# Optimization experiments

Hardware: AMD Instinct MI355X
Metric: run time of the kernel (lower is better)

Reference implementation:

```python
import jax, jax.numpy as jnp
import numpy as np

Z_DIMS = (64, 64, 64, 64)
B, T = 16, 1024
IN_CH, CH = 512, 2048
M = 1024
D = sum(Z_DIMS)
LN_EPS = 1e-5
COMMIT = 0.25


def setup_inputs() -> dict:
    key = jax.random.key(0)
    ks = jax.random.split(key, 4)
    x = jax.random.normal(ks[0], (B, T, IN_CH), jnp.float32)
    masks = jnp.ones((B, T), jnp.float32)
    W1 = jax.random.normal(ks[1], (IN_CH, CH), jnp.float32) / np.sqrt(IN_CH).astype(np.float32)
    ln_g = jnp.ones((CH,), jnp.float32)
    ln_b = jnp.zeros((CH,), jnp.float32)
    W2 = jax.random.normal(ks[2], (CH, D), jnp.float32) / np.sqrt(CH).astype(np.float32)
    b2 = jnp.zeros((D,), jnp.float32)
    # Dirichlet(alpha=100) rows are near-uniform positive distributions per head block;
    # emulate with a low-temperature softmax so each z_dim block sums to 1 per row.
    emb_parts = [jax.nn.softmax(0.1 * jax.random.normal(jax.random.fold_in(ks[3], i), (M, d), jnp.float32), axis=-1)
                 for i, d in enumerate(Z_DIMS)]
    embedding = jnp.concatenate(emb_parts, axis=-1)  # [M, D]
    return {"x": x, "masks": masks, "W1": W1, "ln_g": ln_g, "ln_b": ln_b,
            "W2": W2, "b2": b2, "embedding": embedding}


def _forward(x, masks, W1, ln_g, ln_b, W2, b2, embedding):
    # Encoder: Linear(no bias) -> LayerNorm -> ReLU -> Linear
    h = x @ W1                                   # [B,T,CH]
    mu = h.mean(-1, keepdims=True)
    var = h.var(-1, keepdims=True)               # biased variance (torch LayerNorm)
    h = (h - mu) / jnp.sqrt(var + LN_EPS) * ln_g + ln_b
    h = jax.nn.relu(h)
    z = h @ W2 + b2                              # [B,T,D]

    # Per-head log_softmax over z_dims slices, concatenated
    parts, start = [], 0
    for d in Z_DIMS:
        parts.append(jax.nn.log_softmax(z[..., start:start + d], axis=-1))
        start += d
    p = jnp.concatenate(parts, axis=-1)          # [B,T,D] log-probs

    # Codebook (eval mode; EMA buffer updates skipped): nearest code under
    # KL(target=p || input=embedding) = sum_d e^{p_d} (p_d - log e_{m,d}).
    # Decompose the broadcast [N,M,D] reduction into a GEMM-friendly form.
    x_flat = jax.lax.stop_gradient(p).reshape(-1, D)   # [N,D]
    ex = jnp.exp(x_flat)
    self_term = jnp.sum(ex * x_flat, axis=-1, keepdims=True)   # [N,1]
    div = self_term - ex @ jnp.log(embedding).T                # [N,M]
    indices = jnp.argmin(div, axis=-1)                          # [N]
    quantized = embedding[indices].reshape(p.shape)             # [B,T,D]
    q_det = jax.lax.stop_gradient(quantized)

    # Commitment loss: masked KL(p || quantized.detach()), mean over batch, sum over time
    kl = jnp.sum(jnp.exp(p) * (p - jnp.log(q_det)), axis=-1)    # [B,T]
    loss = COMMIT * jnp.sum(jnp.mean(kl * masks, axis=0))

    # Straight-through estimator
    q_st = p + jax.lax.stop_gradient(quantized - p)
    return z, q_st, loss


def reference(x, masks, W1, ln_g, ln_b, W2, b2, embedding):
    return _forward(x, masks, W1, ln_g, ln_b, W2, b2, embedding)
```

## Files before the change

### kernel.cpp

```cpp
#include <hip/hip_runtime.h>
#include <math.h>

#define NROWS 16384
#define INCH  512
#define CH    2048
#define DD    256
#define MM    1024

typedef unsigned short u16;
typedef short short8 __attribute__((ext_vector_type(8)));
typedef float f32x4 __attribute__((ext_vector_type(4)));

__device__ __forceinline__ u16 f2bf(float f) {
  unsigned u = __float_as_uint(f);
  return (u16)((u + 0x7fffu + ((u >> 16) & 1u)) >> 16);
}
__device__ __forceinline__ float bf2f(u16 h) {
  return __uint_as_float(((unsigned)h) << 16);
}
__device__ __forceinline__ void gload16(const u16* g, u16* lds) {
  __builtin_amdgcn_global_load_lds((const __attribute__((address_space(1))) void*)g,
                                   (__attribute__((address_space(3))) void*)lds, 16, 0, 0);
}


__global__ __launch_bounds__(256) void k_split_x(const float* __restrict__ x,
                                                 u16* __restrict__ xb) {
  const size_t i = ((size_t)blockIdx.x * 256 + threadIdx.x) * 8;
  float4 a = *(const float4*)(x + i);
  float4 b = *(const float4*)(x + i + 4);
  float v[8] = {a.x, a.y, a.z, a.w, b.x, b.y, b.z, b.w};
  unsigned hw[4];
#pragma unroll
  for (int p = 0; p < 4; ++p)
    hw[p] = (unsigned)f2bf(v[2 * p]) | ((unsigned)f2bf(v[2 * p + 1]) << 16);
  *(uint4*)(xb + i) = make_uint4(hw[0], hw[1], hw[2], hw[3]);
}

__global__ __launch_bounds__(256) void k_split_wT(const float* __restrict__ src,
                                                  u16* __restrict__ dh, int R, int C) {
  __shared__ float t[32][33];
  const int tx = threadIdx.x & 31, ty = threadIdx.x >> 5;
  const int c0 = blockIdx.x * 32, r0 = blockIdx.y * 32;
#pragma unroll
  for (int i = 0; i < 4; ++i)
    t[ty + i * 8][tx] = src[(size_t)(r0 + ty + i * 8) * C + c0 + tx];
  __syncthreads();
#pragma unroll
  for (int i = 0; i < 4; ++i) {
    float v = t[tx][ty + i * 8];
    dh[(size_t)(c0 + ty + i * 8) * R + r0 + tx] = f2bf(v);
  }
}

__global__ __launch_bounds__(256) void k_gemm1(const u16* __restrict__ Xb,
                                               const u16* __restrict__ W1ht,
                                               u16* __restrict__ Hh,
                                               float* __restrict__ STATS) {
  __shared__ u16 sm[2][1024 * 8];
  const int tid = threadIdx.x;
  const int lane = tid & 63, w = tid >> 6;
  const int wr = w >> 1, wc = w & 1;
  const int hw = blockIdx.x;
  const int u = hw >> 3;
  const int by = (hw & 7) * 16 + (u >> 4);
  const int bx = u & 15;
  const int gm = by * 128, n0 = bx * 128;

  f32x4 acc[4][4];
#pragma unroll
  for (int i = 0; i < 4; ++i)
#pragma unroll
    for (int j = 0; j < 4; ++j) acc[i][j] = (f32x4){0.f, 0.f, 0.f, 0.f};

  auto STAGE = [&](int buf, int kt) {
#pragma unroll
    for (int t = 0; t < 4; ++t) {
      const int f = t * 256 + tid;
      const int isB = f >> 9;
      const int wi = f & 511;
      const int grp = wi >> 6, s2 = wi & 63;
      const int row = (isB ? n0 : gm) + grp * 16 + (s2 >> 2);
      const int k16 = (s2 & 3) ^ ((s2 >> 3) & 3);
      const u16* src = isB ? W1ht : Xb;
      gload16(src + ((size_t)row << 9) + (kt << 5) + k16 * 8,
              &sm[buf][(size_t)f * 8]);
    }
  };

  STAGE(0, 0);
  const int lr = lane & 15;
  const int rI = lr * 4 + ((lane >> 4) ^ ((lr >> 1) & 3));
  for (int kt = 0; kt < 16; ++kt) {
    __syncthreads();
    if (kt + 1 < 16) STAGE((kt + 1) & 1, kt + 1);
    const u16* base = sm[kt & 1];
    short8 bh[4];
#pragma unroll
    for (int j = 0; j < 4; ++j)
      bh[j] = *(const short8*)(base + (size_t)(512 + (wc * 4 + j) * 64 + rI) * 8);
#pragma unroll
    for (int i = 0; i < 4; ++i) {
      short8 ah = *(const short8*)(base + (size_t)((wr * 4 + i) * 64 + rI) * 8);
#pragma unroll
      for (int j = 0; j < 4; ++j)
        acc[i][j] = __builtin_amdgcn_mfma_f32_16x16x32_bf16(ah, bh[j], acc[i][j], 0, 0, 0);
    }
  }

  float* smf = (float*)&sm[0][0];
  const int rr = (lane >> 4) << 2, cc = lane & 15;
  const int lrow = tid >> 3, cg = tid & 7;
#pragma unroll
  for (int s = 0; s < 4; ++s) {
    __syncthreads();
    if (wr == (s >> 1)) {
#pragma unroll
      for (int ii = 0; ii < 2; ++ii) {
        const int i = (s & 1) * 2 + ii;
#pragma unroll
        for (int j = 0; j < 4; ++j)
#pragma unroll
          for (int reg = 0; reg < 4; ++reg)
            smf[(ii * 16 + rr + reg) * 132 + wc * 64 + j * 16 + cc] = acc[i][j][reg];
      }
    }
    __syncthreads();
    const int grow = gm + s * 32 + lrow;
    float s1 = 0.f, ss = 0.f;
    float v[16];
#pragma unroll
    for (int q = 0; q < 4; ++q)
      *(f32x4*)&v[q * 4] = *(const f32x4*)&smf[lrow * 132 + cg * 16 + q * 4];
#pragma unroll
    for (int e = 0; e < 16; ++e) { s1 += v[e]; ss += v[e] * v[e]; }
    unsigned hw2[8];
#pragma unroll
    for (int p = 0; p < 8; ++p) {
      const u16 h0 = f2bf(v[2 * p]), h1 = f2bf(v[2 * p + 1]);
      hw2[p] = (unsigned)h0 | ((unsigned)h1 << 16);
    }
    const size_t o = (size_t)grow * CH + n0 + cg * 16;
    *(uint4*)&Hh[o] = make_uint4(hw2[0], hw2[1], hw2[2], hw2[3]);
    *(uint4*)&Hh[o + 8] = make_uint4(hw2[4], hw2[5], hw2[6], hw2[7]);
#pragma unroll
    for (int m = 1; m <= 4; m <<= 1) { s1 += __shfl_xor(s1, m); ss += __shfl_xor(ss, m); }
    if (cg == 0)
      *(float2*)&STATS[(size_t)grow * 32 + bx * 2] = make_float2(s1, ss);
  }
}

__global__ __launch_bounds__(256) void k_rowstats(const float* __restrict__ STATS,
                                                  float2* __restrict__ MU2) {
  const int row = blockIdx.x * 256 + threadIdx.x;
  float s = 0.f, ss = 0.f;
#pragma unroll
  for (int i = 0; i < 16; ++i) {
    float2 p = *(const float2*)&STATS[((size_t)row << 5) + i * 2];
    s += p.x; ss += p.y;
  }
  const float mu = s * (1.f / CH);
  const float var = ss * (1.f / CH) - mu * mu;
  MU2[row] = make_float2(mu, 1.f / sqrtf(var + 1e-5f));
}

__global__ __launch_bounds__(512) void k_gemm2(const u16* __restrict__ Hh,
                                               const u16* __restrict__ W2ht,
                                               const float* __restrict__ lng, const float* __restrict__ lnb,
                                               const float2* __restrict__ MU2,
                                               const float* __restrict__ b2,
                                               float* __restrict__ Z,
                                               u16* __restrict__ EXh,
                                               float* __restrict__ SELF) {
  __shared__ u16 sm[2][1280 * 8];
  __shared__ float selfp[64][4];
  const int tid = threadIdx.x;
  const int lane = tid & 63, w = tid >> 6;
  const int wr = w >> 2, wc = w & 3;
  const int gm = blockIdx.x * 64;
  const int st_row = lane >> 2;
  const int st_k16 = (lane & 3) ^ ((lane >> 3) & 3);

  const int arow = tid >> 2, akc = tid & 3;
  const int pcA = (arow >> 4) * 64 + (arow & 15) * 4 + (akc ^ ((arow >> 1) & 3));
  float2 murv = make_float2(0.f, 0.f);
  const u16* gHh = nullptr;
  if (tid < 256) {
    murv = MU2[gm + arow];
    gHh = Hh + ((size_t)(gm + arow) << 11) + akc * 8;
  }

  f32x4 acc[2][4];
#pragma unroll
  for (int i = 0; i < 2; ++i)
#pragma unroll
    for (int j = 0; j < 4; ++j) acc[i][j] = (f32x4){0.f, 0.f, 0.f, 0.f};

  uint4 hwreg;
  auto A_LOAD = [&](int kt) {
    if (tid < 256) hwreg = *(const uint4*)(gHh + kt * 32);
  };
  auto B_STAGE = [&](int buf, int kt) {
    if (w >= 4) {
#pragma unroll
      for (int t = 0; t < 4; ++t) {
        const int f = (w - 4) * 256 + t * 64 + lane;
        const int grp = f >> 6;
        const int row = grp * 16 + st_row;
        gload16(W2ht + ((size_t)row << 11) + (kt << 5) + st_k16 * 8,
                &sm[buf][(size_t)(256 + f) * 8]);
      }
    }
  };
  auto LN_WRITE = [&](int buf, int kt) {
    if (tid < 256) {
      const int kb = kt * 32 + akc * 8;
      float4 g0 = *(const float4*)&lng[kb];
      float4 g1 = *(const float4*)&lng[kb + 4];
      float4 bb0 = *(const float4*)&lnb[kb];
      float4 bb1 = *(const float4*)&lnb[kb + 4];
      const float gg[8] = {g0.x, g0.y, g0.z, g0.w, g1.x, g1.y, g1.z, g1.w};
      const float bb[8] = {bb0.x, bb0.y, bb0.z, bb0.w, bb1.x, bb1.y, bb1.z, bb1.w};
      const unsigned hws[4] = {hwreg.x, hwreg.y, hwreg.z, hwreg.w};
      unsigned oh[4];
#pragma unroll
      for (int p = 0; p < 4; ++p) {
        u16 yh[2];
#pragma unroll
        for (int e = 0; e < 2; ++e) {
          const float h = bf2f((u16)(hws[p] >> (16 * e)));
          const float a1 = murv.y * gg[2 * p + e];
          const float y = fmaxf(fmaf(h, a1, bb[2 * p + e] - murv.x * a1), 0.f);
          yh[e] = f2bf(y);
        }
        oh[p] = (unsigned)yh[0] | ((unsigned)yh[1] << 16);
      }
      *(uint4*)&sm[buf][(size_t)pcA * 8] = make_uint4(oh[0], oh[1], oh[2], oh[3]);
    }
  };

  const int lr = lane & 15;
  const int rI = lr * 4 + ((lane >> 4) ^ ((lr >> 1) & 3));

  A_LOAD(0);
  B_STAGE(0, 0);
  LN_WRITE(0, 0);

  for (int kt = 0; kt < 64; ++kt) {
    __syncthreads();
    if (kt + 1 < 64) {
      A_LOAD(kt + 1);
      B_STAGE((kt + 1) & 1, kt + 1);
    }
    const u16* base = sm[kt & 1];
    short8 ah[2], bh[4];
#pragma unroll
    for (int i = 0; i < 2; ++i)
      ah[i] = *(const short8*)(base + ((wr * 2 + i) * 64 + rI) * 8);
#pragma unroll
    for (int j = 0; j < 4; ++j)
      bh[j] = *(const short8*)(base + (256 + (wc * 4 + j) * 64 + rI) * 8);
#pragma unroll
    for (int i = 0; i < 2; ++i)
#pragma unroll
      for (int j = 0; j < 4; ++j)
        acc[i][j] = __builtin_amdgcn_mfma_f32_16x16x32_bf16(ah[i], bh[j], acc[i][j], 0, 0, 0);
    if (kt + 1 < 64) LN_WRITE((kt + 1) & 1, kt + 1);
  }

  const int cc = lane & 15;
  float bias[4];
#pragma unroll
  for (int j = 0; j < 4; ++j) bias[j] = b2[wc * 64 + j * 16 + cc];

#pragma unroll
  for (int i = 0; i < 2; ++i)
#pragma unroll
    for (int reg = 0; reg < 4; ++reg) {
      const int rl = wr * 32 + i * 16 + ((lane >> 4) << 2) + reg;
      const int row = gm + rl;
      float z[4];
#pragma unroll
      for (int j = 0; j < 4; ++j) z[j] = acc[i][j][reg] + bias[j];
      float mx = fmaxf(fmaxf(z[0], z[1]), fmaxf(z[2], z[3]));
#pragma unroll
      for (int m = 1; m <= 8; m <<= 1) mx = fmaxf(mx, __shfl_xor(mx, m));
      float se = expf(z[0] - mx) + expf(z[1] - mx) + expf(z[2] - mx) + expf(z[3] - mx);
#pragma unroll
      for (int m = 1; m <= 8; m <<= 1) se += __shfl_xor(se, m);
      const float lse = mx + logf(se);
      float selfc = 0.f;
#pragma unroll
      for (int j = 0; j < 4; ++j) {
        const float p = z[j] - lse;
        const float e = expf(p);
        selfc += e * p;
        const size_t o = (size_t)row * DD + wc * 64 + j * 16 + cc;
        Z[o] = z[j];
        EXh[o] = f2bf(e);
      }
#pragma unroll
      for (int m = 1; m <= 8; m <<= 1) selfc += __shfl_xor(selfc, m);
      if (cc == 0) selfp[rl][wc] = selfc;
    }
  __syncthreads();
  if (tid < 64)
    SELF[gm + tid] = selfp[tid][0] + selfp[tid][1] + selfp[tid][2] + selfp[tid][3];
}

__global__ __launch_bounds__(256) void k_prep_le(const float* __restrict__ E,
                                                 u16* __restrict__ LEh) {
  const size_t i = ((size_t)blockIdx.x * 256 + threadIdx.x) * 4;
  float4 v4 = *(const float4*)&E[i];
  const u16 h0 = f2bf(logf(v4.x)), h1 = f2bf(logf(v4.y));
  const u16 h2 = f2bf(logf(v4.z)), h3 = f2bf(logf(v4.w));
  *(uint2*)&LEh[i] = make_uint2((unsigned)h0 | ((unsigned)h1 << 16),
                                (unsigned)h2 | ((unsigned)h3 << 16));
}

__global__ __launch_bounds__(256) void k_dots(const u16* __restrict__ EXh,
                                              const u16* __restrict__ LEh,
                                              float* __restrict__ PV, int* __restrict__ PI) {
  __shared__ u16 sm[2][1024 * 8];
  const int tid = threadIdx.x;
  const int lane = tid & 63, w = tid >> 6;
  const int wr = w >> 1, wc = w & 1;
  const int hw = blockIdx.x;
  const int by = (hw & 7) * 16 + (hw >> 6);
  const int bx = (hw >> 3) & 7;
  const int gm = by * 128, m0 = bx * 128;

  f32x4 acc[4][4];
#pragma unroll
  for (int i = 0; i < 4; ++i)
#pragma unroll
    for (int j = 0; j < 4; ++j) acc[i][j] = (f32x4){0.f, 0.f, 0.f, 0.f};

  auto STAGE = [&](int buf, int kt) {
#pragma unroll
    for (int t = 0; t < 4; ++t) {
      const int f = t * 256 + tid;
      const int mtx = f >> 9;
      const int wi = f & 511;
      const int grp = wi >> 6, s2 = wi & 63;
      const int rowbase = mtx ? m0 : gm;
      const int row = rowbase + grp * 16 + (s2 >> 2);
      const int k16 = (s2 & 3) ^ ((s2 >> 3) & 3);
      const u16* src = mtx ? LEh : EXh;
      gload16(src + ((size_t)row << 8) + (kt << 5) + k16 * 8,
              &sm[buf][(size_t)f * 8]);
    }
  };

  STAGE(0, 0);
  const int rI = (lane & 15) * 4 + ((lane >> 4) ^ ((lane >> 1) & 3));
  for (int kt = 0; kt < 8; ++kt) {
    __syncthreads();
    if (kt + 1 < 8) STAGE((kt + 1) & 1, kt + 1);
    const u16* base = sm[kt & 1];
    short8 eh[4], bh[4];
#pragma unroll
    for (int i = 0; i < 4; ++i) {
      eh[i] = *(const short8*)(base + ((wr * 4 + i) * 64 + rI) * 8);
      bh[i] = *(const short8*)(base + (512 + (wc * 4 + i) * 64 + rI) * 8);
    }
#pragma unroll
    for (int i = 0; i < 4; ++i)
#pragma unroll
      for (int j = 0; j < 4; ++j)
        acc[i][j] = __builtin_amdgcn_mfma_f32_16x16x32_bf16(eh[i], bh[j], acc[i][j], 0, 0, 0);
  }

  const int cc = lane & 15;
  const int mtile = bx * 2 + wc;
#pragma unroll
  for (int i = 0; i < 4; ++i)
#pragma unroll
    for (int reg = 0; reg < 4; ++reg) {
      float bv = acc[i][0][reg];
      int bi = m0 + wc * 64 + cc;
#pragma unroll
      for (int j = 1; j < 4; ++j) {
        const float v = acc[i][j][reg];
        if (v > bv) { bv = v; bi = m0 + wc * 64 + j * 16 + cc; }
      }
#pragma unroll
      for (int msk = 8; msk; msk >>= 1) {
        const float ov = __shfl_xor(bv, msk);
        const int   oi = __shfl_xor(bi, msk);
        if (ov > bv || (ov == bv && oi < bi)) { bv = ov; bi = oi; }
      }
      if (cc == 0) {
        const int row = gm + wr * 64 + i * 16 + ((lane >> 4) << 2) + reg;
        PV[row * 16 + mtile] = bv;
        PI[row * 16 + mtile] = bi;
      }
    }
}

__global__ __launch_bounds__(256) void k_scan(const float* __restrict__ PV,
                                              const int* __restrict__ PI,
                                              const float* __restrict__ SELF,
                                              const float* __restrict__ E,
                                              float* __restrict__ Q,
                                              float* __restrict__ KL) {
  const int tid = threadIdx.x;
  const int lane = tid & 63;
  const int row = blockIdx.x * 4 + (tid >> 6);

  float bv = -1e30f;
  int bi = 0x7fffffff;
  if (lane < 16) { bv = PV[row * 16 + lane]; bi = PI[row * 16 + lane]; }
#pragma unroll
  for (int m = 32; m; m >>= 1) {
    const float ov = __shfl_xor(bv, m);
    const int   oi = __shfl_xor(bi, m);
    if (ov > bv || (ov == bv && oi < bi)) { bv = ov; bi = oi; }
  }
  if (lane == 0) KL[row] = SELF[row] - bv;
  float4 e4 = *(const float4*)&E[((size_t)bi << 8) + lane * 4];
  *(float4*)&Q[((size_t)row << 8) + lane * 4] = e4;
}

__global__ __launch_bounds__(256) void k_loss(const float* __restrict__ KL,
                                              const float* __restrict__ MASK,
                                              float* __restrict__ out) {
  __shared__ float red[4];
  const int tid = threadIdx.x;
  float s = 0.f;
  for (int i = tid; i < NROWS; i += 256) s += KL[i] * MASK[i];
#pragma unroll
  for (int m = 32; m; m >>= 1) s += __shfl_xor(s, m);
  if ((tid & 63) == 0) red[tid >> 6] = s;
  __syncthreads();
  if (tid == 0) out[0] = (red[0] + red[1] + red[2] + red[3]) * (0.25f / 16.f);
}

extern "C" void kernel_launch(void* const* d_in, const int* in_sizes, int n_in,
                              void* d_out, int out_size, void* d_ws, size_t ws_size,
                              hipStream_t stream) {
  const float* x     = (const float*)d_in[0];
  const float* masks = (const float*)d_in[1];
  const float* W1    = (const float*)d_in[2];
  const float* ln_g  = (const float*)d_in[3];
  const float* ln_b  = (const float*)d_in[4];
  const float* W2    = (const float*)d_in[5];
  const float* b2    = (const float*)d_in[6];
  const float* emb   = (const float*)d_in[7];

  float* z_out = (float*)d_out;
  float* q_out = z_out + (size_t)NROWS * DD;
  float* loss_out = z_out + 2 * (size_t)NROWS * DD;

  char* ws = (char*)d_ws;
  u16*   Hh   = (u16*)(ws);
  u16*   W1ht = (u16*)(ws + 67108864);
  u16*   W2ht = (u16*)(ws + 69206016);
  u16*   LEh  = (u16*)(ws + 70254592);
  float* SELF = (float*)(ws + 70778880);
  float* KL   = (float*)(ws + 70844416);
  float2* MU2 = (float2*)(ws + 70909952);
  u16*   Xb   = (u16*)(ws + 71041024);
  float* PV   = (float*)(ws);
  int*   PI   = (int*)(ws + 1048576);
  float* STATS = (float*)q_out;
  u16*   EXh  = (u16*)q_out;

  k_split_x<<<(NROWS * INCH) / 2048, 256, 0, stream>>>(x, Xb);
  k_split_wT<<<dim3(64, 16), 256, 0, stream>>>(W1, W1ht, INCH, CH);
  k_split_wT<<<dim3(8, 64), 256, 0, stream>>>(W2, W2ht, CH, DD);
  k_prep_le<<<256, 256, 0, stream>>>(emb, LEh);

  k_gemm1<<<2048, 256, 0, stream>>>(Xb, W1ht, Hh, STATS);
  k_rowstats<<<NROWS / 256, 256, 0, stream>>>(STATS, MU2);
  k_gemm2<<<NROWS / 64, 512, 0, stream>>>(Hh, W2ht, ln_g, ln_b, MU2, b2,
                                          z_out, EXh, SELF);

  k_dots<<<1024, 256, 0, stream>>>(EXh, LEh, PV, PI);
  k_scan<<<4096, 256, 0, stream>>>(PV, PI, SELF, emb, q_out, KL);
  k_loss<<<1, 256, 0, stream>>>(KL, masks, loss_out);
}
```

Baseline: 192.7 us.

## Split gemm2 across N halves and apply LayerNorm in registers after LDS load

The second GEMM is now launched on a 2D grid. Each 256-thread block computes 128 of the 256 output columns, which doubles the number of blocks. The A tile is now staged straight into LDS with async global-to-LDS loads, and LayerNorm+ReLU is applied to the MFMA fragments in registers. This replaces the old path where some threads loaded, normalized and wrote A to LDS. The self-entropy term becomes two partial sums per row that k_scan adds together. As a result, each column-half block recomputes the normalization and reloads the H rows.

New measurement: 200.1 us. 3.8% more time.

```diff
diff --git a/kernel.cpp b/kernel.cpp
--- a/kernel.cpp
+++ b/kernel.cpp
@@ -164,31 +164,36 @@
   MU2[row] = make_float2(mu, 1.f / sqrtf(var + 1e-5f));
 }
 
-__global__ __launch_bounds__(512) void k_gemm2(const u16* __restrict__ Hh,
+__global__ __launch_bounds__(256) void k_gemm2(const u16* __restrict__ Hh,
                                                const u16* __restrict__ W2ht,
                                                const float* __restrict__ lng, const float* __restrict__ lnb,
                                                const float2* __restrict__ MU2,
                                                const float* __restrict__ b2,
                                                float* __restrict__ Z,
                                                u16* __restrict__ EXh,
-                                               float* __restrict__ SELF) {
-  __shared__ u16 sm[2][1280 * 8];
-  __shared__ float selfp[64][4];
+                                               float* __restrict__ SELF2) {
+  __shared__ u16 sm[2][768 * 8];
+  __shared__ float selfp[64][2];
   const int tid = threadIdx.x;
   const int lane = tid & 63, w = tid >> 6;
-  const int wr = w >> 2, wc = w & 3;
+  const int wr = w >> 1, wc = w & 1;
   const int gm = blockIdx.x * 64;
-  const int st_row = lane >> 2;
-  const int st_k16 = (lane & 3) ^ ((lane >> 3) & 3);
-
-  const int arow = tid >> 2, akc = tid & 3;
-  const int pcA = (arow >> 4) * 64 + (arow & 15) * 4 + (akc ^ ((arow >> 1) & 3));
-  float2 murv = make_float2(0.f, 0.f);
-  const u16* gHh = nullptr;
-  if (tid < 256) {
-    murv = MU2[gm + arow];
-    gHh = Hh + ((size_t)(gm + arow) << 11) + akc * 8;
-  }
+  const int n0 = blockIdx.y * 128;
+
+  auto STAGE = [&](int buf, int kt) {
+#pragma unroll
+    for (int t = 0; t < 3; ++t) {
+      const int f = t * 256 + tid;
+      const int isB = (f >= 256);
+      const int wi = isB ? (f - 256) : f;
+      const int grp = wi >> 6, s2 = wi & 63;
+      const int row = (isB ? n0 : gm) + grp * 16 + (s2 >> 2);
+      const int k16 = (s2 & 3) ^ ((s2 >> 3) & 3);
+      const u16* src = isB ? W2ht : Hh;
+      gload16(src + ((size_t)row << 11) + (kt << 5) + k16 * 8,
+              &sm[buf][(size_t)f * 8]);
+    }
+  };
 
   f32x4 acc[2][4];
 #pragma unroll
@@ -196,82 +201,52 @@
 #pragma unroll
     for (int j = 0; j < 4; ++j) acc[i][j] = (f32x4){0.f, 0.f, 0.f, 0.f};
 
-  uint4 hwreg;
-  auto A_LOAD = [&](int kt) {
-    if (tid < 256) hwreg = *(const uint4*)(gHh + kt * 32);
-  };
-  auto B_STAGE = [&](int buf, int kt) {
-    if (w >= 4) {
-#pragma unroll
-      for (int t = 0; t < 4; ++t) {
-        const int f = (w - 4) * 256 + t * 64 + lane;
-        const int grp = f >> 6;
-        const int row = grp * 16 + st_row;
-        gload16(W2ht + ((size_t)row << 11) + (kt << 5) + st_k16 * 8,
-                &sm[buf][(size_t)(256 + f) * 8]);
-      }
-    }
-  };
-  auto LN_WRITE = [&](int buf, int kt) {
-    if (tid < 256) {
-      const int kb = kt * 32 + akc * 8;
-      float4 g0 = *(const float4*)&lng[kb];
-      float4 g1 = *(const float4*)&lng[kb + 4];
-      float4 bb0 = *(const float4*)&lnb[kb];
-      float4 bb1 = *(const float4*)&lnb[kb + 4];
-      const float gg[8] = {g0.x, g0.y, g0.z, g0.w, g1.x, g1.y, g1.z, g1.w};
-      const float bb[8] = {bb0.x, bb0.y, bb0.z, bb0.w, bb1.x, bb1.y, bb1.z, bb1.w};
-      const unsigned hws[4] = {hwreg.x, hwreg.y, hwreg.z, hwreg.w};
-      unsigned oh[4];
-#pragma unroll
-      for (int p = 0; p < 4; ++p) {
-        u16 yh[2];
-#pragma unroll
-        for (int e = 0; e < 2; ++e) {
-          const float h = bf2f((u16)(hws[p] >> (16 * e)));
-          const float a1 = murv.y * gg[2 * p + e];
-          const float y = fmaxf(fmaf(h, a1, bb[2 * p + e] - murv.x * a1), 0.f);
-          yh[e] = f2bf(y);
-        }
-        oh[p] = (unsigned)yh[0] | ((unsigned)yh[1] << 16);
-      }
-      *(uint4*)&sm[buf][(size_t)pcA * 8] = make_uint4(oh[0], oh[1], oh[2], oh[3]);
-    }
-  };
-
-  const int lr = lane & 15;
-  const int rI = lr * 4 + ((lane >> 4) ^ ((lr >> 1) & 3));
-
-  A_LOAD(0);
-  B_STAGE(0, 0);
-  LN_WRITE(0, 0);
-
+  const int lr = lane & 15, kc2 = lane >> 4;
+  const int rI = lr * 4 + (kc2 ^ ((lr >> 1) & 3));
+  const float2 mrow[2] = {MU2[gm + wr * 32 + lr], MU2[gm + wr * 32 + 16 + lr]};
+
+  STAGE(0, 0);
   for (int kt = 0; kt < 64; ++kt) {
     __syncthreads();
-    if (kt + 1 < 64) {
-      A_LOAD(kt + 1);
-      B_STAGE((kt + 1) & 1, kt + 1);
-    }
+    if (kt + 1 < 64) STAGE((kt + 1) & 1, kt + 1);
     const u16* base = sm[kt & 1];
-    short8 ah[2], bh[4];
+    short8 ar[2], bh[4];
 #pragma unroll
     for (int i = 0; i < 2; ++i)
-      ah[i] = *(const short8*)(base + ((wr * 2 + i) * 64 + rI) * 8);
+      ar[i] = *(const short8*)(base + ((wr * 2 + i) * 64 + rI) * 8);
 #pragma unroll
     for (int j = 0; j < 4; ++j)
       bh[j] = *(const short8*)(base + (256 + (wc * 4 + j) * 64 + rI) * 8);
+    const int kb = kt * 32 + kc2 * 8;
+    float4 g0 = *(const float4*)&lng[kb];
+    float4 g1 = *(const float4*)&lng[kb + 4];
+    float4 b0 = *(const float4*)&lnb[kb];
+    float4 b1 = *(const float4*)&lnb[kb + 4];
+    const float gg[8] = {g0.x, g0.y, g0.z, g0.w, g1.x, g1.y, g1.z, g1.w};
+    const float bb[8] = {b0.x, b0.y, b0.z, b0.w, b1.x, b1.y, b1.z, b1.w};
+    short8 ah[2];
+#pragma unroll
+    for (int i = 0; i < 2; ++i) {
+      const float2 mu = mrow[i];
+#pragma unroll
+      for (int e = 0; e < 8; ++e) {
+        const float h = bf2f((u16)ar[i][e]);
+        const float a1 = mu.y * gg[e];
+        const float y = fmaxf(fmaf(h, a1, bb[e] - mu.x * a1), 0.f);
+        ah[i][e] = (short)f2bf(y);
+      }
+    }
 #pragma unroll
     for (int i = 0; i < 2; ++i)
 #pragma unroll
       for (int j = 0; j < 4; ++j)
         acc[i][j] = __builtin_amdgcn_mfma_f32_16x16x32_bf16(ah[i], bh[j], acc[i][j], 0, 0, 0);
-    if (kt + 1 < 64) LN_WRITE((kt + 1) & 1, kt + 1);
   }
 
   const int cc = lane & 15;
   float bias[4];
 #pragma unroll
-  for (int j = 0; j < 4; ++j) bias[j] = b2[wc * 64 + j * 16 + cc];
+  for (int j = 0; j < 4; ++j) bias[j] = b2[n0 + wc * 64 + j * 16 + cc];
 
 #pragma unroll
   for (int i = 0; i < 2; ++i)
@@ -295,7 +270,7 @@
         const float p = z[j] - lse;
         const float e = expf(p);
         selfc += e * p;
-        const size_t o = (size_t)row * DD + wc * 64 + j * 16 + cc;
+        const size_t o = (size_t)row * DD + n0 + wc * 64 + j * 16 + cc;
         Z[o] = z[j];
         EXh[o] = f2bf(e);
       }
@@ -305,7 +280,7 @@
     }
   __syncthreads();
   if (tid < 64)
-    SELF[gm + tid] = selfp[tid][0] + selfp[tid][1] + selfp[tid][2] + selfp[tid][3];
+    SELF2[(size_t)(gm + tid) * 2 + blockIdx.y] = selfp[tid][0] + selfp[tid][1];
 }
 
 __global__ __launch_bounds__(256) void k_prep_le(const float* __restrict__ E,
@@ -400,7 +375,7 @@
 
 __global__ __launch_bounds__(256) void k_scan(const float* __restrict__ PV,
                                               const int* __restrict__ PI,
-                                              const float* __restrict__ SELF,
+                                              const float* __restrict__ SELF2,
                                               const float* __restrict__ E,
                                               float* __restrict__ Q,
                                               float* __restrict__ KL) {
@@ -417,7 +392,7 @@
     const int   oi = __shfl_xor(bi, m);
     if (ov > bv || (ov == bv && oi < bi)) { bv = ov; bi = oi; }
   }
-  if (lane == 0) KL[row] = SELF[row] - bv;
+  if (lane == 0) KL[row] = SELF2[(size_t)row * 2] + SELF2[(size_t)row * 2 + 1] - bv;
   float4 e4 = *(const float4*)&E[((size_t)bi << 8) + lane * 4];
   *(float4*)&Q[((size_t)row << 8) + lane * 4] = e4;
 }
@@ -453,18 +428,18 @@
   float* loss_out = z_out + 2 * (size_t)NROWS * DD;
 
   char* ws = (char*)d_ws;
-  u16*   Hh   = (u16*)(ws);
-  u16*   W1ht = (u16*)(ws + 67108864);
-  u16*   W2ht = (u16*)(ws + 69206016);
-  u16*   LEh  = (u16*)(ws + 70254592);
-  float* SELF = (float*)(ws + 70778880);
-  float* KL   = (float*)(ws + 70844416);
-  float2* MU2 = (float2*)(ws + 70909952);
-  u16*   Xb   = (u16*)(ws + 71041024);
-  float* PV   = (float*)(ws);
-  int*   PI   = (int*)(ws + 1048576);
+  u16*   Hh    = (u16*)(ws);
+  u16*   W1ht  = (u16*)(ws + 67108864);
+  u16*   W2ht  = (u16*)(ws + 69206016);
+  u16*   LEh   = (u16*)(ws + 70254592);
+  float* SELF2 = (float*)(ws + 70778880);
+  float* KL    = (float*)(ws + 70909952);
+  float2* MU2  = (float2*)(ws + 70975488);
+  u16*   Xb    = (u16*)(ws + 71106560);
+  float* PV    = (float*)(ws);
+  int*   PI    = (int*)(ws + 1048576);
   float* STATS = (float*)q_out;
-  u16*   EXh  = (u16*)q_out;
+  u16*   EXh   = (u16*)q_out;
 
   k_split_x<<<(NROWS * INCH) / 2048, 256, 0, stream>>>(x, Xb);
   k_split_wT<<<dim3(64, 16), 256, 0, stream>>>(W1, W1ht, INCH, CH);
@@ -473,10 +448,10 @@
 
   k_gemm1<<<2048, 256, 0, stream>>>(Xb, W1ht, Hh, STATS);
   k_rowstats<<<NROWS / 256, 256, 0, stream>>>(STATS, MU2);
-  k_gemm2<<<NROWS / 64, 512, 0, stream>>>(Hh, W2ht, ln_g, ln_b, MU2, b2,
-                                          z_out, EXh, SELF);
+  k_gemm2<<<dim3(NROWS / 64, 2), 256, 0, stream>>>(Hh, W2ht, ln_g, ln_b, MU2, b2,
+                                                   z_out, EXh, SELF2);
 
   k_dots<<<1024, 256, 0, stream>>>(EXh, LEh, PV, PI);
-  k_scan<<<4096, 256, 0, stream>>>(PV, PI, SELF, emb, q_out, KL);
+  k_scan<<<4096, 256, 0, stream>>>(PV, PI, SELF2, emb, q_out, KL);
   k_loss<<<1, 256, 0, stream>>>(KL, masks, loss_out);
 }
```
